# Kernel tuning notes

Measured on AMD Instinct MI355X. Metric: run time of the kernel, lower is better.

Reference implementation:

```python
import jax, jax.numpy as jnp
import numpy as np

B, N, DIN, DOUT = 4, 4096, 512, 128
NEG_INF = -1.0e9  # matches torch's -1000000000.0 fill


def setup_inputs() -> dict:
    key = jax.random.key(0)
    k1, k2, k3, k4 = jax.random.split(key, 4)
    x = jax.random.normal(k1, (B, N, DIN), dtype=jnp.float32)
    adj = (jax.random.uniform(k2, (N, N)) < 0.004).astype(jnp.float32)
    # xavier_uniform with gain=sqrt(2) for weights
    lim_w = float(np.sqrt(2.0) * np.sqrt(6.0 / (DIN + DOUT)))
    weights = jax.random.uniform(k3, (DIN, DOUT), jnp.float32, -lim_w, lim_w)
    # xavier_uniform (gain=1) for a: shape [2*DOUT, 1]
    lim_a = float(np.sqrt(6.0 / (2 * DOUT + 1)))
    a = jax.random.uniform(k4, (2 * DOUT, 1), jnp.float32, -lim_a, lim_a)
    return {"x": x, "adj": adj, "weights": weights, "a": a}


def reference(x, adj, weights, a):
    d = weights.shape[1]
    a_src = a[:d]   # [D, 1]
    a_dst = a[d:]   # [D, 1]

    def per_graph(xs):  # xs: [N, DIN]
        wh = xs @ weights                      # [N, D]
        e = wh @ a_src + (wh @ a_dst).T        # [N,1] + [1,N] -> [N,N]
        e = jnp.where(e > 0, e, 0.01 * e)      # LeakyReLU(0.01)
        att = jax.nn.softmax(jnp.where(adj > 0, e, NEG_INF), axis=1)
        out = att @ wh                          # [N, D]
        return adj @ out                        # sparse-adj mm (dense here)

    return jax.nn.relu(jax.vmap(per_graph)(x))  # act = ReLU
```

## Files before the change

kernel.cpp:

```cpp
#include <hip/hip_runtime.h>
#include <hip/hip_bf16.h>
#include <cstdint>
#include <cstddef>

#define BATCH 4
#define NNODE 4096
#define DIN   512
#define DOUT  128
#define CAP   64

typedef __attribute__((ext_vector_type(8))) short bf16x8;
typedef __attribute__((ext_vector_type(4))) float f32x4;

static __device__ __forceinline__ unsigned short f2bf_rne(float f) {
    union { float f; uint32_t u; } v; v.f = f;
    uint32_t u = v.u;
    uint32_t r = u + 0x7FFFu + ((u >> 16) & 1u);
    return (unsigned short)(r >> 16);
}
static __device__ __forceinline__ float bf2f(unsigned short h) {
    union { float f; uint32_t u; } v; v.u = ((uint32_t)h) << 16;
    return v.f;
}

__global__ __launch_bounds__(256) void k_build_csr(const float* __restrict__ adj,
                                                   int* __restrict__ nbr_cnt,
                                                   int* __restrict__ nbr_idx) {
    __shared__ int pref[256];
    int row = blockIdx.x;
    int t = threadIdx.x;
    const float4* p = (const float4*)(adj + (size_t)row * NNODE) + t * 4;
    unsigned mask = 0;
#pragma unroll
    for (int q = 0; q < 4; ++q) {
        float4 v = p[q];
        mask |= (v.x > 0.f ? 1u : 0u) << (q*4+0);
        mask |= (v.y > 0.f ? 1u : 0u) << (q*4+1);
        mask |= (v.z > 0.f ? 1u : 0u) << (q*4+2);
        mask |= (v.w > 0.f ? 1u : 0u) << (q*4+3);
    }
    int cnt = __popc(mask);
    pref[t] = cnt;
    __syncthreads();
    for (int off = 1; off < 256; off <<= 1) {
        int v = pref[t];
        int add = (t >= off) ? pref[t - off] : 0;
        __syncthreads();
        pref[t] = v + add;
        __syncthreads();
    }
    int total = pref[255];
    int base = pref[t] - cnt;
    int cbase = t * 16;
    while (mask) {
        int b = __ffs(mask) - 1;
        mask &= mask - 1;
        if (base < CAP) nbr_idx[row * CAP + base] = cbase + b;
        ++base;
    }
    if (t == 0) nbr_cnt[row] = total > CAP ? CAP : total;
}

__global__ __launch_bounds__(256) void k_wt(const float* __restrict__ W,
                                            unsigned short* __restrict__ Wt) {
    __shared__ float tile[32][33];
    int kb = (blockIdx.x >> 2) * 32;
    int nb = (blockIdx.x & 3) * 32;
    int t = threadIdx.x;
#pragma unroll
    for (int r = 0; r < 4; ++r) {
        int kl = r*8 + (t >> 5);
        int nl = t & 31;
        tile[kl][nl] = W[(size_t)(kb+kl)*DOUT + nb+nl];
    }
    __syncthreads();
#pragma unroll
    for (int r = 0; r < 4; ++r) {
        int nl = r*8 + (t >> 5);
        int kl = t & 31;
        Wt[(size_t)(nb+nl)*DIN + kb+kl] = f2bf_rne(tile[kl][nl]);
    }
}

__global__ __launch_bounds__(256) void k_wh(const float* __restrict__ x,
                                            const unsigned short* __restrict__ Wt,
                                            const float* __restrict__ a,
                                            float* __restrict__ wh,
                                            float* __restrict__ sv,
                                            float* __restrict__ dvv) {
    __shared__ float lacc[2][8][64][4];
    int w = threadIdx.x >> 6;
    int l = threadIdx.x & 63;
    int g = w >> 1;
    int h = w & 1;
    int rowbase = blockIdx.x * 32 + g * 16;
    int row = rowbase + (l & 15);
    int kq = (l >> 4) * 8;
    f32x4 acc[8] = {};
    const float* xrow = x + (size_t)row * DIN + h*256 + kq;
    const unsigned short* wbase = Wt + h*256 + kq;
    for (int ks = 0; ks < 8; ++ks) {
        float4 a0 = *(const float4*)(xrow + ks*32);
        float4 a1 = *(const float4*)(xrow + ks*32 + 4);
        float af[8] = {a0.x,a0.y,a0.z,a0.w,a1.x,a1.y,a1.z,a1.w};
        bf16x8 ah, al;
#pragma unroll
        for (int i = 0; i < 8; ++i) {
            unsigned short hh = f2bf_rne(af[i]);
            ah[i] = (short)hh;
            al[i] = (short)f2bf_rne(af[i] - bf2f(hh));
        }
#pragma unroll
        for (int ni = 0; ni < 8; ++ni) {
            bf16x8 b = *(const bf16x8*)(wbase + (size_t)(ni*16 + (l & 15))*DIN + ks*32);
            acc[ni] = __builtin_amdgcn_mfma_f32_16x16x32_bf16(ah, b, acc[ni], 0, 0, 0);
            acc[ni] = __builtin_amdgcn_mfma_f32_16x16x32_bf16(al, b, acc[ni], 0, 0, 0);
        }
    }
    if (h == 1) {
#pragma unroll
        for (int ni = 0; ni < 8; ++ni)
            *(f32x4*)&lacc[g][ni][l][0] = acc[ni];
    }
    __syncthreads();
    if (h == 0) {
#pragma unroll
        for (int ni = 0; ni < 8; ++ni) {
            f32x4 o = *(const f32x4*)&lacc[g][ni][l][0];
            acc[ni] += o;
        }
        float sp[4] = {0,0,0,0}, dp[4] = {0,0,0,0};
#pragma unroll
        for (int ni = 0; ni < 8; ++ni) {
            int col = ni*16 + (l & 15);
            float as = a[col];
            float ad = a[DOUT + col];
#pragma unroll
            for (int r = 0; r < 4; ++r) {
                sp[r] += acc[ni][r] * as;
                dp[r] += acc[ni][r] * ad;
            }
        }
#pragma unroll
        for (int off = 1; off <= 8; off <<= 1) {
#pragma unroll
            for (int r = 0; r < 4; ++r) {
                sp[r] += __shfl_xor(sp[r], off, 64);
                dp[r] += __shfl_xor(dp[r], off, 64);
            }
        }
        int row4 = rowbase + (l >> 4) * 4;
        if ((l & 15) == 0) {
#pragma unroll
            for (int r = 0; r < 4; ++r) {
                sv[row4 + r] = sp[r];
                dvv[row4 + r] = dp[r];
            }
        }
#pragma unroll
        for (int ni = 0; ni < 8; ++ni) {
            int col = ni*16 + (l & 15);
#pragma unroll
            for (int r = 0; r < 4; ++r)
                wh[(size_t)(row4 + r)*DOUT + col] = acc[ni][r];
        }
    }
}

__global__ __launch_bounds__(128) void k_colsum(const float* __restrict__ wh,
                                                float* __restrict__ colsum) {
    int b = blockIdx.x >> 7;
    int chunk = blockIdx.x & 127;
    int col = threadIdx.x;
    const float* base = wh + ((size_t)b*NNODE + chunk*32)*DOUT + col;
    float sum = 0.f;
    for (int r = 0; r < 32; ++r) sum += base[(size_t)r*DOUT];
    atomicAdd(&colsum[b*DOUT + col], sum);
}

__global__ __launch_bounds__(256) void k_att(const float* __restrict__ wh,
                                             const float* __restrict__ s,
                                             const float* __restrict__ dv,
                                             const int* __restrict__ nbr_cnt,
                                             const int* __restrict__ nbr_idx,
                                             const float* __restrict__ colsum,
                                             float* __restrict__ out) {
    int gid = blockIdx.x*4 + (threadIdx.x >> 6);
    int l = threadIdx.x & 63;
    int b = gid >> 12;
    int i = gid & (NNODE-1);
    int c = nbr_cnt[i];
    int j = (l < c) ? nbr_idx[i*CAP + l] : 0;
    float e = -3.0e38f;
    float si = s[gid];
    if (l < c) {
        float ev = si + dv[(b << 12) + j];
        e = ev > 0.f ? ev : 0.01f * ev;
    }
    float m = e;
#pragma unroll
    for (int off = 32; off >= 1; off >>= 1) m = fmaxf(m, __shfl_xor(m, off, 64));
    float p = (l < c) ? __expf(e - m) : 0.f;
    float den = p;
#pragma unroll
    for (int off = 32; off >= 1; off >>= 1) den += __shfl_xor(den, off, 64);
    int half = l >> 5;
    int lc = l & 31;
    float4 acc = {0.f, 0.f, 0.f, 0.f};
    if (c > 0) {
        float inv = 1.f / den;
        for (int jj = 0; jj < c; jj += 2) {
            int src = jj + half;
            int jv = __shfl(j, src, 64);
            float pv = __shfl(p, src, 64) * inv;
            float4 v = *((const float4*)(wh + ((size_t)((b << 12) + jv))*DOUT) + lc);
            acc.x += pv * v.x; acc.y += pv * v.y;
            acc.z += pv * v.z; acc.w += pv * v.w;
        }
        acc.x += __shfl_xor(acc.x, 32, 64);
        acc.y += __shfl_xor(acc.y, 32, 64);
        acc.z += __shfl_xor(acc.z, 32, 64);
        acc.w += __shfl_xor(acc.w, 32, 64);
    } else {
        const float inv_n = 1.f / (float)NNODE;
        acc.x = colsum[(b << 7) + lc*4]     * inv_n;
        acc.y = colsum[(b << 7) + lc*4 + 1] * inv_n;
        acc.z = colsum[(b << 7) + lc*4 + 2] * inv_n;
        acc.w = colsum[(b << 7) + lc*4 + 3] * inv_n;
    }
    if (half == 0)
        *((float4*)(out + (size_t)gid*DOUT) + lc) = acc;
}

__global__ __launch_bounds__(256) void k_agg(const float* __restrict__ out,
                                             const int* __restrict__ nbr_cnt,
                                             const int* __restrict__ nbr_idx,
                                             float* __restrict__ y) {
    int gid = blockIdx.x*4 + (threadIdx.x >> 6);
    int l = threadIdx.x & 63;
    int b = gid >> 12;
    int i = gid & (NNODE-1);
    int c = nbr_cnt[i];
    int j = (l < c) ? nbr_idx[i*CAP + l] : 0;
    int half = l >> 5;
    int lc = l & 31;
    float4 acc = {0.f, 0.f, 0.f, 0.f};
    for (int jj = 0; jj < c; jj += 2) {
        int src = jj + half;
        if (src < c) {
            int jv = __shfl(j, src, 64);
            float4 v = *((const float4*)(out + ((size_t)((b << 12) + jv))*DOUT) + lc);
            acc.x += v.x; acc.y += v.y; acc.z += v.z; acc.w += v.w;
        }
    }
    acc.x += __shfl_xor(acc.x, 32, 64);
    acc.y += __shfl_xor(acc.y, 32, 64);
    acc.z += __shfl_xor(acc.z, 32, 64);
    acc.w += __shfl_xor(acc.w, 32, 64);
    acc.x = fmaxf(acc.x, 0.f); acc.y = fmaxf(acc.y, 0.f);
    acc.z = fmaxf(acc.z, 0.f); acc.w = fmaxf(acc.w, 0.f);
    if (half == 0)
        *((float4*)(y + (size_t)gid*DOUT) + lc) = acc;
}

extern "C" void kernel_launch(void* const* d_in, const int* in_sizes, int n_in,
                              void* d_out, int out_size, void* d_ws, size_t ws_size,
                              hipStream_t stream) {
    const float* x   = (const float*)d_in[0];
    const float* adj = (const float*)d_in[1];
    const float* W   = (const float*)d_in[2];
    const float* a   = (const float*)d_in[3];
    float* y = (float*)d_out;

    char* ws = (char*)d_ws;
    size_t o = 0;
    int*            nbr_cnt = (int*)(ws + o);            o += (size_t)NNODE*4;
    int*            nbr_idx = (int*)(ws + o);            o += (size_t)NNODE*CAP*4;
    unsigned short* Wt      = (unsigned short*)(ws + o); o += (size_t)DOUT*DIN*2;
    float*          wh      = (float*)(ws + o);          o += (size_t)BATCH*NNODE*DOUT*4;
    float*          sv      = (float*)(ws + o);          o += (size_t)BATCH*NNODE*4;
    float*          dvv     = (float*)(ws + o);          o += (size_t)BATCH*NNODE*4;
    float*          colsum  = (float*)(ws + o);          o += (size_t)BATCH*DOUT*4;
    float*          outbuf  = (float*)(ws + o);          o += (size_t)BATCH*NNODE*DOUT*4;

    hipMemsetAsync(colsum, 0, (size_t)BATCH*DOUT*4, stream);

    k_build_csr<<<NNODE, 256, 0, stream>>>(adj, nbr_cnt, nbr_idx);
    k_wt<<<64, 256, 0, stream>>>(W, Wt);
    k_wh<<<(BATCH*NNODE)/32, 256, 0, stream>>>(x, Wt, a, wh, sv, dvv);
    k_colsum<<<BATCH*128, 128, 0, stream>>>(wh, colsum);
    k_att<<<(BATCH*NNODE)/4, 256, 0, stream>>>(wh, sv, dvv, nbr_cnt, nbr_idx, colsum, outbuf);
    k_agg<<<(BATCH*NNODE)/4, 256, 0, stream>>>(outbuf, nbr_cnt, nbr_idx, y);
}
```

Before: 182.0 us.

## Fuse all stages into one cooperative persistent kernel with grid syncs

Replaces the six launches and memset with one cooperative kernel that uses grid-wide syncs between phases. Half the blocks compute the projection while the other half build the CSR neighbour lists at the same time. Column sums are folded into the projection epilogue with atomics, and the K split goes from two waves to four. This removes launch gaps and the separate column-sum pass. In exchange it pays grid-sync costs, a persistent grid sized from occupancy, and heavier atomic traffic on colsum.

```diff
diff --git a/kernel.cpp b/kernel.cpp
--- a/kernel.cpp
+++ b/kernel.cpp
@@ -1,13 +1,16 @@
 #include <hip/hip_runtime.h>
-#include <hip/hip_bf16.h>
+#include <hip/hip_cooperative_groups.h>
 #include <cstdint>
 #include <cstddef>
+
+namespace cg = cooperative_groups;
 
 #define BATCH 4
 #define NNODE 4096
 #define DIN   512
 #define DOUT  128
 #define CAP   64
+#define NGROUP 1024
 
 typedef __attribute__((ext_vector_type(8))) short bf16x8;
 typedef __attribute__((ext_vector_type(4))) float f32x4;
@@ -23,244 +26,228 @@
     return v.f;
 }
 
-__global__ __launch_bounds__(256) void k_build_csr(const float* __restrict__ adj,
-                                                   int* __restrict__ nbr_cnt,
-                                                   int* __restrict__ nbr_idx) {
-    __shared__ int pref[256];
-    int row = blockIdx.x;
-    int t = threadIdx.x;
-    const float4* p = (const float4*)(adj + (size_t)row * NNODE) + t * 4;
-    unsigned mask = 0;
-#pragma unroll
-    for (int q = 0; q < 4; ++q) {
-        float4 v = p[q];
-        mask |= (v.x > 0.f ? 1u : 0u) << (q*4+0);
-        mask |= (v.y > 0.f ? 1u : 0u) << (q*4+1);
-        mask |= (v.z > 0.f ? 1u : 0u) << (q*4+2);
-        mask |= (v.w > 0.f ? 1u : 0u) << (q*4+3);
-    }
-    int cnt = __popc(mask);
-    pref[t] = cnt;
-    __syncthreads();
-    for (int off = 1; off < 256; off <<= 1) {
-        int v = pref[t];
-        int add = (t >= off) ? pref[t - off] : 0;
-        __syncthreads();
-        pref[t] = v + add;
-        __syncthreads();
-    }
-    int total = pref[255];
-    int base = pref[t] - cnt;
-    int cbase = t * 16;
-    while (mask) {
-        int b = __ffs(mask) - 1;
-        mask &= mask - 1;
-        if (base < CAP) nbr_idx[row * CAP + base] = cbase + b;
-        ++base;
-    }
-    if (t == 0) nbr_cnt[row] = total > CAP ? CAP : total;
-}
-
-__global__ __launch_bounds__(256) void k_wt(const float* __restrict__ W,
-                                            unsigned short* __restrict__ Wt) {
-    __shared__ float tile[32][33];
-    int kb = (blockIdx.x >> 2) * 32;
-    int nb = (blockIdx.x & 3) * 32;
-    int t = threadIdx.x;
-#pragma unroll
-    for (int r = 0; r < 4; ++r) {
-        int kl = r*8 + (t >> 5);
-        int nl = t & 31;
-        tile[kl][nl] = W[(size_t)(kb+kl)*DOUT + nb+nl];
-    }
-    __syncthreads();
-#pragma unroll
-    for (int r = 0; r < 4; ++r) {
-        int nl = r*8 + (t >> 5);
-        int kl = t & 31;
-        Wt[(size_t)(nb+nl)*DIN + kb+kl] = f2bf_rne(tile[kl][nl]);
-    }
-}
-
-__global__ __launch_bounds__(256) void k_wh(const float* __restrict__ x,
-                                            const unsigned short* __restrict__ Wt,
-                                            const float* __restrict__ a,
-                                            float* __restrict__ wh,
-                                            float* __restrict__ sv,
-                                            float* __restrict__ dvv) {
-    __shared__ float lacc[2][8][64][4];
-    int w = threadIdx.x >> 6;
-    int l = threadIdx.x & 63;
-    int g = w >> 1;
-    int h = w & 1;
-    int rowbase = blockIdx.x * 32 + g * 16;
-    int row = rowbase + (l & 15);
-    int kq = (l >> 4) * 8;
-    f32x4 acc[8] = {};
-    const float* xrow = x + (size_t)row * DIN + h*256 + kq;
-    const unsigned short* wbase = Wt + h*256 + kq;
-    for (int ks = 0; ks < 8; ++ks) {
-        float4 a0 = *(const float4*)(xrow + ks*32);
-        float4 a1 = *(const float4*)(xrow + ks*32 + 4);
-        float af[8] = {a0.x,a0.y,a0.z,a0.w,a1.x,a1.y,a1.z,a1.w};
-        bf16x8 ah, al;
-#pragma unroll
-        for (int i = 0; i < 8; ++i) {
-            unsigned short hh = f2bf_rne(af[i]);
-            ah[i] = (short)hh;
-            al[i] = (short)f2bf_rne(af[i] - bf2f(hh));
-        }
-#pragma unroll
-        for (int ni = 0; ni < 8; ++ni) {
-            bf16x8 b = *(const bf16x8*)(wbase + (size_t)(ni*16 + (l & 15))*DIN + ks*32);
-            acc[ni] = __builtin_amdgcn_mfma_f32_16x16x32_bf16(ah, b, acc[ni], 0, 0, 0);
-            acc[ni] = __builtin_amdgcn_mfma_f32_16x16x32_bf16(al, b, acc[ni], 0, 0, 0);
-        }
-    }
-    if (h == 1) {
-#pragma unroll
-        for (int ni = 0; ni < 8; ++ni)
-            *(f32x4*)&lacc[g][ni][l][0] = acc[ni];
-    }
-    __syncthreads();
-    if (h == 0) {
-#pragma unroll
-        for (int ni = 0; ni < 8; ++ni) {
-            f32x4 o = *(const f32x4*)&lacc[g][ni][l][0];
-            acc[ni] += o;
-        }
-        float sp[4] = {0,0,0,0}, dp[4] = {0,0,0,0};
-#pragma unroll
-        for (int ni = 0; ni < 8; ++ni) {
-            int col = ni*16 + (l & 15);
-            float as = a[col];
-            float ad = a[DOUT + col];
-#pragma unroll
-            for (int r = 0; r < 4; ++r) {
-                sp[r] += acc[ni][r] * as;
-                dp[r] += acc[ni][r] * ad;
-            }
-        }
-#pragma unroll
-        for (int off = 1; off <= 8; off <<= 1) {
-#pragma unroll
-            for (int r = 0; r < 4; ++r) {
-                sp[r] += __shfl_xor(sp[r], off, 64);
-                dp[r] += __shfl_xor(dp[r], off, 64);
-            }
-        }
-        int row4 = rowbase + (l >> 4) * 4;
-        if ((l & 15) == 0) {
-#pragma unroll
-            for (int r = 0; r < 4; ++r) {
-                sv[row4 + r] = sp[r];
-                dvv[row4 + r] = dp[r];
-            }
-        }
-#pragma unroll
-        for (int ni = 0; ni < 8; ++ni) {
-            int col = ni*16 + (l & 15);
-#pragma unroll
-            for (int r = 0; r < 4; ++r)
-                wh[(size_t)(row4 + r)*DOUT + col] = acc[ni][r];
-        }
-    }
-}
-
-__global__ __launch_bounds__(128) void k_colsum(const float* __restrict__ wh,
-                                                float* __restrict__ colsum) {
-    int b = blockIdx.x >> 7;
-    int chunk = blockIdx.x & 127;
-    int col = threadIdx.x;
-    const float* base = wh + ((size_t)b*NNODE + chunk*32)*DOUT + col;
-    float sum = 0.f;
-    for (int r = 0; r < 32; ++r) sum += base[(size_t)r*DOUT];
-    atomicAdd(&colsum[b*DOUT + col], sum);
-}
-
-__global__ __launch_bounds__(256) void k_att(const float* __restrict__ wh,
-                                             const float* __restrict__ s,
-                                             const float* __restrict__ dv,
-                                             const int* __restrict__ nbr_cnt,
-                                             const int* __restrict__ nbr_idx,
-                                             const float* __restrict__ colsum,
-                                             float* __restrict__ out) {
-    int gid = blockIdx.x*4 + (threadIdx.x >> 6);
-    int l = threadIdx.x & 63;
-    int b = gid >> 12;
-    int i = gid & (NNODE-1);
-    int c = nbr_cnt[i];
-    int j = (l < c) ? nbr_idx[i*CAP + l] : 0;
-    float e = -3.0e38f;
-    float si = s[gid];
-    if (l < c) {
-        float ev = si + dv[(b << 12) + j];
-        e = ev > 0.f ? ev : 0.01f * ev;
-    }
-    float m = e;
-#pragma unroll
-    for (int off = 32; off >= 1; off >>= 1) m = fmaxf(m, __shfl_xor(m, off, 64));
-    float p = (l < c) ? __expf(e - m) : 0.f;
-    float den = p;
-#pragma unroll
-    for (int off = 32; off >= 1; off >>= 1) den += __shfl_xor(den, off, 64);
-    int half = l >> 5;
-    int lc = l & 31;
-    float4 acc = {0.f, 0.f, 0.f, 0.f};
-    if (c > 0) {
-        float inv = 1.f / den;
-        for (int jj = 0; jj < c; jj += 2) {
-            int src = jj + half;
-            int jv = __shfl(j, src, 64);
-            float pv = __shfl(p, src, 64) * inv;
-            float4 v = *((const float4*)(wh + ((size_t)((b << 12) + jv))*DOUT) + lc);
-            acc.x += pv * v.x; acc.y += pv * v.y;
-            acc.z += pv * v.z; acc.w += pv * v.w;
-        }
-        acc.x += __shfl_xor(acc.x, 32, 64);
-        acc.y += __shfl_xor(acc.y, 32, 64);
-        acc.z += __shfl_xor(acc.z, 32, 64);
-        acc.w += __shfl_xor(acc.w, 32, 64);
+__global__ __launch_bounds__(256, 4) void k_mega(
+    const float* __restrict__ x, const float* __restrict__ adj,
+    const float* __restrict__ W, const float* __restrict__ a,
+    float* __restrict__ y,
+    int* __restrict__ nbr_cnt, int* __restrict__ nbr_idx,
+    unsigned short* __restrict__ Wt, float* __restrict__ wh,
+    float* __restrict__ sv, float* __restrict__ dvv,
+    float* __restrict__ colsum, float* __restrict__ outbuf)
+{
+    cg::grid_group grid = cg::this_grid();
+    __shared__ float lacc[3][8][64][4];
+    __shared__ int scnt;
+
+    const int nb = gridDim.x;
+    const int t  = threadIdx.x;
+    const int w  = t >> 6;
+    const int l  = t & 63;
+
+    for (int i = blockIdx.x * 256 + t; i < DOUT * DIN; i += nb * 256) {
+        int n = i >> 9;
+        int k = i & (DIN - 1);
+        Wt[i] = f2bf_rne(W[(size_t)k * DOUT + n]);
+    }
+    for (int i = blockIdx.x * 256 + t; i < BATCH * DOUT; i += nb * 256)
+        colsum[i] = 0.f;
+    grid.sync();
+
+    const int nc = nb >> 1;
+    if (blockIdx.x < nc) {
+        for (int g = blockIdx.x; g < NGROUP; g += nc) {
+            int rowbase = g * 16;
+            int row = rowbase + (l & 15);
+            int kq = w * 128 + ((l >> 4) << 3);
+            f32x4 acc[8] = {};
+            const float* xrow = x + (size_t)row * DIN + kq;
+            const unsigned short* wb = Wt + kq;
+#pragma unroll
+            for (int ks = 0; ks < 4; ++ks) {
+                float4 a0 = *(const float4*)(xrow + ks * 32);
+                float4 a1 = *(const float4*)(xrow + ks * 32 + 4);
+                float af[8] = {a0.x,a0.y,a0.z,a0.w,a1.x,a1.y,a1.z,a1.w};
+                bf16x8 ah, al;
+#pragma unroll
+                for (int i2 = 0; i2 < 8; ++i2) {
+                    unsigned short hh = f2bf_rne(af[i2]);
+                    ah[i2] = (short)hh;
+                    al[i2] = (short)f2bf_rne(af[i2] - bf2f(hh));
+                }
+#pragma unroll
+                for (int ni = 0; ni < 8; ++ni) {
+                    bf16x8 b = *(const bf16x8*)(wb + (size_t)(ni*16 + (l & 15)) * DIN + ks * 32);
+                    acc[ni] = __builtin_amdgcn_mfma_f32_16x16x32_bf16(ah, b, acc[ni], 0, 0, 0);
+                    acc[ni] = __builtin_amdgcn_mfma_f32_16x16x32_bf16(al, b, acc[ni], 0, 0, 0);
+                }
+            }
+            if (w > 0) {
+#pragma unroll
+                for (int ni = 0; ni < 8; ++ni)
+                    *(f32x4*)&lacc[w-1][ni][l][0] = acc[ni];
+            }
+            __syncthreads();
+            if (w == 0) {
+#pragma unroll
+                for (int ni = 0; ni < 8; ++ni) {
+                    acc[ni] += *(const f32x4*)&lacc[0][ni][l][0];
+                    acc[ni] += *(const f32x4*)&lacc[1][ni][l][0];
+                    acc[ni] += *(const f32x4*)&lacc[2][ni][l][0];
+                }
+                float sp[4] = {0,0,0,0}, dp[4] = {0,0,0,0};
+#pragma unroll
+                for (int ni = 0; ni < 8; ++ni) {
+                    int col = ni*16 + (l & 15);
+                    float as = a[col], ad = a[DOUT + col];
+#pragma unroll
+                    for (int r = 0; r < 4; ++r) {
+                        sp[r] += acc[ni][r] * as;
+                        dp[r] += acc[ni][r] * ad;
+                    }
+                }
+#pragma unroll
+                for (int off = 1; off <= 8; off <<= 1) {
+#pragma unroll
+                    for (int r = 0; r < 4; ++r) {
+                        sp[r] += __shfl_xor(sp[r], off, 64);
+                        dp[r] += __shfl_xor(dp[r], off, 64);
+                    }
+                }
+                int row4 = rowbase + ((l >> 4) << 2);
+                if ((l & 15) == 0) {
+#pragma unroll
+                    for (int r = 0; r < 4; ++r) {
+                        sv[row4 + r] = sp[r];
+                        dvv[row4 + r] = dp[r];
+                    }
+                }
+                int bidx = rowbase >> 12;
+#pragma unroll
+                for (int ni = 0; ni < 8; ++ni) {
+                    int col = ni*16 + (l & 15);
+                    atomicAdd(&colsum[(bidx << 7) + col],
+                              acc[ni][0] + acc[ni][1] + acc[ni][2] + acc[ni][3]);
+#pragma unroll
+                    for (int r = 0; r < 4; ++r)
+                        wh[(size_t)(row4 + r) * DOUT + col] = acc[ni][r];
+                }
+            }
+            __syncthreads();
+        }
     } else {
-        const float inv_n = 1.f / (float)NNODE;
-        acc.x = colsum[(b << 7) + lc*4]     * inv_n;
-        acc.y = colsum[(b << 7) + lc*4 + 1] * inv_n;
-        acc.z = colsum[(b << 7) + lc*4 + 2] * inv_n;
-        acc.w = colsum[(b << 7) + lc*4 + 3] * inv_n;
-    }
-    if (half == 0)
-        *((float4*)(out + (size_t)gid*DOUT) + lc) = acc;
-}
-
-__global__ __launch_bounds__(256) void k_agg(const float* __restrict__ out,
-                                             const int* __restrict__ nbr_cnt,
-                                             const int* __restrict__ nbr_idx,
-                                             float* __restrict__ y) {
-    int gid = blockIdx.x*4 + (threadIdx.x >> 6);
-    int l = threadIdx.x & 63;
-    int b = gid >> 12;
-    int i = gid & (NNODE-1);
-    int c = nbr_cnt[i];
-    int j = (l < c) ? nbr_idx[i*CAP + l] : 0;
-    int half = l >> 5;
-    int lc = l & 31;
-    float4 acc = {0.f, 0.f, 0.f, 0.f};
-    for (int jj = 0; jj < c; jj += 2) {
-        int src = jj + half;
-        if (src < c) {
-            int jv = __shfl(j, src, 64);
-            float4 v = *((const float4*)(out + ((size_t)((b << 12) + jv))*DOUT) + lc);
-            acc.x += v.x; acc.y += v.y; acc.z += v.z; acc.w += v.w;
-        }
-    }
-    acc.x += __shfl_xor(acc.x, 32, 64);
-    acc.y += __shfl_xor(acc.y, 32, 64);
-    acc.z += __shfl_xor(acc.z, 32, 64);
-    acc.w += __shfl_xor(acc.w, 32, 64);
-    acc.x = fmaxf(acc.x, 0.f); acc.y = fmaxf(acc.y, 0.f);
-    acc.z = fmaxf(acc.z, 0.f); acc.w = fmaxf(acc.w, 0.f);
-    if (half == 0)
-        *((float4*)(y + (size_t)gid*DOUT) + lc) = acc;
+        const int nA = nb - nc;
+        for (int row = blockIdx.x - nc; row < NNODE; row += nA) {
+            if (t == 0) scnt = 0;
+            __syncthreads();
+            const float4* p = (const float4*)(adj + (size_t)row * NNODE) + t * 4;
+            unsigned mask = 0;
+#pragma unroll
+            for (int q = 0; q < 4; ++q) {
+                float4 v = p[q];
+                mask |= (v.x > 0.f ? 1u : 0u) << (q*4+0);
+                mask |= (v.y > 0.f ? 1u : 0u) << (q*4+1);
+                mask |= (v.z > 0.f ? 1u : 0u) << (q*4+2);
+                mask |= (v.w > 0.f ? 1u : 0u) << (q*4+3);
+            }
+            int cnt = __popc(mask);
+            int base = cnt ? atomicAdd(&scnt, cnt) : 0;
+            int cbase = t * 16;
+            while (mask) {
+                int bit = __ffs(mask) - 1;
+                mask &= mask - 1;
+                if (base < CAP) nbr_idx[row * CAP + base] = cbase + bit;
+                ++base;
+            }
+            __syncthreads();
+            if (t == 0) nbr_cnt[row] = scnt > CAP ? CAP : scnt;
+        }
+    }
+    grid.sync();
+
+    {
+        int gwave = blockIdx.x * 4 + w;
+        for (int u = gwave; u < 4096; u += nb * 4) {
+            for (int rr = 0; rr < 4; ++rr) {
+                int gid = u * 4 + rr;
+                int b = gid >> 12;
+                int i = gid & (NNODE - 1);
+                int c = nbr_cnt[i];
+                int j = (l < c) ? nbr_idx[i * CAP + l] : 0;
+                float e = -3.0e38f;
+                float si = sv[gid];
+                if (l < c) {
+                    float ev = si + dvv[(b << 12) + j];
+                    e = ev > 0.f ? ev : 0.01f * ev;
+                }
+                float m = e;
+#pragma unroll
+                for (int off = 32; off >= 1; off >>= 1) m = fmaxf(m, __shfl_xor(m, off, 64));
+                float pp = (l < c) ? __expf(e - m) : 0.f;
+                float den = pp;
+#pragma unroll
+                for (int off = 32; off >= 1; off >>= 1) den += __shfl_xor(den, off, 64);
+                int half = l >> 5;
+                int lc = l & 31;
+                float4 acc = {0.f, 0.f, 0.f, 0.f};
+                if (c > 0) {
+                    float inv = 1.f / den;
+                    for (int jj = 0; jj < c; jj += 2) {
+                        int src = jj + half;
+                        int jv = __shfl(j, src, 64);
+                        float pv = __shfl(pp, src, 64) * inv;
+                        float4 v = *((const float4*)(wh + ((size_t)((b << 12) + jv)) * DOUT) + lc);
+                        acc.x += pv * v.x; acc.y += pv * v.y;
+                        acc.z += pv * v.z; acc.w += pv * v.w;
+                    }
+                    acc.x += __shfl_xor(acc.x, 32, 64);
+                    acc.y += __shfl_xor(acc.y, 32, 64);
+                    acc.z += __shfl_xor(acc.z, 32, 64);
+                    acc.w += __shfl_xor(acc.w, 32, 64);
+                } else {
+                    const float inv_n = 1.f / (float)NNODE;
+                    acc.x = colsum[(b << 7) + lc*4]     * inv_n;
+                    acc.y = colsum[(b << 7) + lc*4 + 1] * inv_n;
+                    acc.z = colsum[(b << 7) + lc*4 + 2] * inv_n;
+                    acc.w = colsum[(b << 7) + lc*4 + 3] * inv_n;
+                }
+                if (half == 0)
+                    *((float4*)(outbuf + (size_t)gid * DOUT) + lc) = acc;
+            }
+        }
+    }
+    grid.sync();
+
+    {
+        int gwave = blockIdx.x * 4 + w;
+        for (int u = gwave; u < 4096; u += nb * 4) {
+            for (int rr = 0; rr < 4; ++rr) {
+                int gid = u * 4 + rr;
+                int b = gid >> 12;
+                int i = gid & (NNODE - 1);
+                int c = nbr_cnt[i];
+                int j = (l < c) ? nbr_idx[i * CAP + l] : 0;
+                int half = l >> 5;
+                int lc = l & 31;
+                float4 acc = {0.f, 0.f, 0.f, 0.f};
+                for (int jj = 0; jj < c; jj += 2) {
+                    int src = jj + half;
+                    if (src < c) {
+                        int jv = __shfl(j, src, 64);
+                        float4 v = *((const float4*)(outbuf + ((size_t)((b << 12) + jv)) * DOUT) + lc);
+                        acc.x += v.x; acc.y += v.y; acc.z += v.z; acc.w += v.w;
+                    }
+                }
+                acc.x += __shfl_xor(acc.x, 32, 64);
+                acc.y += __shfl_xor(acc.y, 32, 64);
+                acc.z += __shfl_xor(acc.z, 32, 64);
+                acc.w += __shfl_xor(acc.w, 32, 64);
+                acc.x = fmaxf(acc.x, 0.f); acc.y = fmaxf(acc.y, 0.f);
+                acc.z = fmaxf(acc.z, 0.f); acc.w = fmaxf(acc.w, 0.f);
+                if (half == 0)
+                    *((float4*)(y + (size_t)gid * DOUT) + lc) = acc;
+            }
+        }
+    }
 }
 
 extern "C" void kernel_launch(void* const* d_in, const int* in_sizes, int n_in,
@@ -274,21 +261,25 @@
 
     char* ws = (char*)d_ws;
     size_t o = 0;
-    int*            nbr_cnt = (int*)(ws + o);            o += (size_t)NNODE*4;
-    int*            nbr_idx = (int*)(ws + o);            o += (size_t)NNODE*CAP*4;
-    unsigned short* Wt      = (unsigned short*)(ws + o); o += (size_t)DOUT*DIN*2;
-    float*          wh      = (float*)(ws + o);          o += (size_t)BATCH*NNODE*DOUT*4;
-    float*          sv      = (float*)(ws + o);          o += (size_t)BATCH*NNODE*4;
-    float*          dvv     = (float*)(ws + o);          o += (size_t)BATCH*NNODE*4;
-    float*          colsum  = (float*)(ws + o);          o += (size_t)BATCH*DOUT*4;
-    float*          outbuf  = (float*)(ws + o);          o += (size_t)BATCH*NNODE*DOUT*4;
-
-    hipMemsetAsync(colsum, 0, (size_t)BATCH*DOUT*4, stream);
-
-    k_build_csr<<<NNODE, 256, 0, stream>>>(adj, nbr_cnt, nbr_idx);
-    k_wt<<<64, 256, 0, stream>>>(W, Wt);
-    k_wh<<<(BATCH*NNODE)/32, 256, 0, stream>>>(x, Wt, a, wh, sv, dvv);
-    k_colsum<<<BATCH*128, 128, 0, stream>>>(wh, colsum);
-    k_att<<<(BATCH*NNODE)/4, 256, 0, stream>>>(wh, sv, dvv, nbr_cnt, nbr_idx, colsum, outbuf);
-    k_agg<<<(BATCH*NNODE)/4, 256, 0, stream>>>(outbuf, nbr_cnt, nbr_idx, y);
-}
+    int*            nbr_cnt = (int*)(ws + o);            o += (size_t)NNODE * 4;
+    int*            nbr_idx = (int*)(ws + o);            o += (size_t)NNODE * CAP * 4;
+    unsigned short* Wt      = (unsigned short*)(ws + o); o += (size_t)DOUT * DIN * 2;
+    float*          wh      = (float*)(ws + o);          o += (size_t)BATCH * NNODE * DOUT * 4;
+    float*          sv      = (float*)(ws + o);          o += (size_t)BATCH * NNODE * 4;
+    float*          dvv     = (float*)(ws + o);          o += (size_t)BATCH * NNODE * 4;
+    float*          colsum  = (float*)(ws + o);          o += (size_t)BATCH * DOUT * 4;
+    float*          outbuf  = (float*)(ws + o);          o += (size_t)BATCH * NNODE * DOUT * 4;
+
+    int occ = 0;
+    hipError_t e = hipOccupancyMaxActiveBlocksPerMultiprocessor(&occ, k_mega, 256, 0);
+    if (e != hipSuccess || occ < 1) occ = 1;
+    long nb = (long)occ * 256;
+    if (nb > 1024) nb = 1024;
+    if (nb < 2) nb = 2;
+
+    void* args[] = {(void*)&x, (void*)&adj, (void*)&W, (void*)&a, (void*)&y,
+                    (void*)&nbr_cnt, (void*)&nbr_idx, (void*)&Wt, (void*)&wh,
+                    (void*)&sv, (void*)&dvv, (void*)&colsum, (void*)&outbuf};
+    hipLaunchCooperativeKernel((void*)k_mega, dim3((uint32_t)nb), dim3(256),
+                               args, 0, stream);
+}
```

After: 539.0 us. 2.96x slower.
